# Kernel optimization log

Hardware: AMD Instinct MI355X
Metric: run time of the kernel (lower is better)

## Reference

```python
import jax, jax.numpy as jnp
import numpy as np

N, C, H, E = 4096, 512, 8, 131072
D = C // H
ALPHA = 0.5
EPS = 1e-5


def layer_norm(x, g, b):
    mu = jnp.mean(x, axis=-1, keepdims=True)
    var = jnp.mean((x - mu) ** 2, axis=-1, keepdims=True)
    return (x - mu) * jax.lax.rsqrt(var + EPS) * g + b


def setup_inputs() -> dict:
    key = jax.random.key(0)
    ks = jax.random.split(key, 20)
    s = 0.02
    return {
        "x": jax.random.normal(ks[0], (N, C), jnp.float32),
        "edge_index": jax.random.randint(ks[1], (2, E), 0, N, jnp.int32),
        "local_w": jax.random.normal(ks[2], (C, C), jnp.float32) * s,
        "local_b": jnp.zeros((C,), jnp.float32),
        "in_proj_w": jax.random.normal(ks[3], (3 * C, C), jnp.float32) * s,
        "in_proj_b": jnp.zeros((3 * C,), jnp.float32),
        "attn_out_w": jax.random.normal(ks[4], (C, C), jnp.float32) * s,
        "attn_out_b": jnp.zeros((C,), jnp.float32),
        "output_w": jax.random.normal(ks[5], (C, C), jnp.float32) * s,
        "output_b": jnp.zeros((C,), jnp.float32),
        "norm1_g": jnp.ones((C,), jnp.float32),
        "norm1_b": jnp.zeros((C,), jnp.float32),
        "norm2_g": jnp.ones((C,), jnp.float32),
        "norm2_b": jnp.zeros((C,), jnp.float32),
        "ffn_w1": jax.random.normal(ks[6], (2 * C, C), jnp.float32) * s,
        "ffn_b1": jnp.zeros((2 * C,), jnp.float32),
        "ffn_w2": jax.random.normal(ks[7], (C, 2 * C), jnp.float32) * s,
        "ffn_b2": jnp.zeros((C,), jnp.float32),
    }


def reference(x, edge_index, local_w, local_b, in_proj_w, in_proj_b,
              attn_out_w, attn_out_b, output_w, output_b,
              norm1_g, norm1_b, norm2_g, norm2_b,
              ffn_w1, ffn_b1, ffn_w2, ffn_b2):
    src, dst = edge_index[0], edge_index[1]

    # local branch: linear then scatter-mean over incoming edges
    local_h = x @ local_w.T + local_b                       # [N,C]
    summed = jax.ops.segment_sum(local_h[src], dst, num_segments=N)
    cnt = jax.ops.segment_sum(jnp.ones((E,), x.dtype), dst, num_segments=N)
    local_out = summed / jnp.maximum(cnt, 1.0)[:, None]

    # global branch: full self-attention over all nodes
    qkv = x @ in_proj_w.T + in_proj_b                       # [N,3C]
    q, k, v = jnp.split(qkv, 3, axis=-1)
    q = q.reshape(N, H, D)
    k = k.reshape(N, H, D)
    v = v.reshape(N, H, D)
    scores = jnp.einsum('nhd,mhd->hnm', q, k) / jnp.sqrt(jnp.asarray(D, x.dtype))
    attn = jax.nn.softmax(scores, axis=-1)                  # [H,N,N]
    ctx = jnp.einsum('hnm,mhd->nhd', attn, v).reshape(N, C)
    global_out = ctx @ attn_out_w.T + attn_out_b

    mixed = ALPHA * local_out + (1.0 - ALPHA) * global_out
    hidden = layer_norm(x + (mixed @ output_w.T + output_b), norm1_g, norm1_b)

    ff = jax.nn.gelu(hidden @ ffn_w1.T + ffn_b1, approximate=False) @ ffn_w2.T + ffn_b2
    return layer_norm(hidden + ff, norm2_g, norm2_b)
```

## Files before the change

### kernel.cpp

```cpp
#include <hip/hip_runtime.h>


#define N_NODES 4096
#define C_DIM   512
#define H_HEADS 8
#define D_HEAD  64
#define E_EDGES 131072

typedef unsigned short u16;
typedef unsigned int   u32;
typedef u16   u16x8  __attribute__((ext_vector_type(8)));
typedef __bf16 bf16x8 __attribute__((ext_vector_type(8)));
typedef float  f32x4  __attribute__((ext_vector_type(4)));

__device__ __forceinline__ float b2f(u16 u) {
  unsigned int i = ((unsigned int)u) << 16;
  return __builtin_bit_cast(float, i);
}
__device__ __forceinline__ u16 f2b(float f) {
  unsigned int i = __builtin_bit_cast(unsigned int, f);
  i += 0x7fffu + ((i >> 16) & 1u);
  return (u16)(i >> 16);
}
__device__ __forceinline__ u16 f2b_up(float f) {
  unsigned int i = __builtin_bit_cast(unsigned int, f);
  return (u16)((i + 0x8000u) >> 16);
}
__device__ __forceinline__ void glds16(const u16* g, u16* l) {
  __builtin_amdgcn_global_load_lds(
      (const __attribute__((address_space(1))) void*)g,
      (__attribute__((address_space(3))) void*)l, 16, 0, 0);
}

struct CvtArgs {
  const float* src[7];
  u16* dst[7];
  int n[7];
  int* deg;
};

__global__ __launch_bounds__(256) void cvt_multi(CvtArgs a) {
  const int t = blockIdx.y;
  if (t == 7) {
    const int i = blockIdx.x * 256 + threadIdx.x;
    if (i < N_NODES) a.deg[i] = 0;
    return;
  }
  const int i = (blockIdx.x * 256 + threadIdx.x) * 8;
  if (i >= a.n[t]) return;
  const float* s = a.src[t] + i;
  f32x4 v0 = *(const f32x4*)s;
  f32x4 v1 = *(const f32x4*)(s + 4);
  u16x8 o;
  o[0]=f2b(v0[0]); o[1]=f2b(v0[1]); o[2]=f2b(v0[2]); o[3]=f2b(v0[3]);
  o[4]=f2b(v1[0]); o[5]=f2b(v1[1]); o[6]=f2b(v1[2]); o[7]=f2b(v1[3]);
  *(u16x8*)(a.dst[t] + i) = o;
}

template<int EPI>
__global__ __launch_bounds__(256) void gemm_bt(
    const u16* __restrict__ A, const u16* __restrict__ W,
    const float* __restrict__ bias, void* __restrict__ outp,
    int M, int Nout, int K,
    const float* __restrict__ mloc)
{
  const int tid  = threadIdx.x;
  const int lane = tid & 63, wave = tid >> 6;
  const int quad = lane >> 4, l16 = lane & 15;
  const int wm = wave >> 1, wn = wave & 1;
  const int bm = blockIdx.x, bnb = blockIdx.y;

  __shared__ __align__(16) u16 As[64][128];
  __shared__ __align__(16) u16 Ws[64][128];

  f32x4 acc[2][2] = {};

  const int lr4 = lane >> 4, gs = lane & 15;
  const int g8e = (gs ^ lr4) * 8;
  const int g8o = (gs ^ (4 + lr4)) * 8;
  const u16* aw[8];
#pragma unroll
  for (int c = 0; c < 4; ++c) {
    const int g8 = (c & 1) ? g8o : g8e;
    aw[c]     = A + (size_t)(bm  * 64 + wave * 16 + c * 4 + lr4) * K + g8;
    aw[4 + c] = W + (size_t)(bnb * 64 + wave * 16 + c * 4 + lr4) * K + g8;
  }

  for (int k0 = 0; k0 < K; k0 += 128) {
    __syncthreads();
#pragma unroll
    for (int c = 0; c < 4; ++c) {
      glds16(aw[c] + k0,     &As[wave * 16 + c * 4][0]);
      glds16(aw[4 + c] + k0, &Ws[wave * 16 + c * 4][0]);
    }
    __syncthreads();
#pragma unroll
    for (int ks = 0; ks < 4; ++ks) {
      const int slot = ((ks * 4 + quad) ^ (l16 & 7)) * 8;
      bf16x8 af[2], bf[2];
      af[0] = *(const bf16x8*)&As[wm * 32 +      l16][slot];
      af[1] = *(const bf16x8*)&As[wm * 32 + 16 + l16][slot];
      bf[0] = *(const bf16x8*)&Ws[wn * 32 +      l16][slot];
      bf[1] = *(const bf16x8*)&Ws[wn * 32 + 16 + l16][slot];
#pragma unroll
      for (int i = 0; i < 2; ++i)
#pragma unroll
        for (int j = 0; j < 2; ++j)
          acc[i][j] = __builtin_amdgcn_mfma_f32_16x16x32_bf16(af[i], bf[j], acc[i][j], 0, 0, 0);
    }
  }

#pragma unroll
  for (int i = 0; i < 2; ++i)
#pragma unroll
    for (int j = 0; j < 2; ++j) {
      const int col = bnb * 64 + wn * 32 + j * 16 + l16;
      const float bias_v = bias[col];
#pragma unroll
      for (int r = 0; r < 4; ++r) {
        const int row = bm * 64 + wm * 32 + i * 16 + quad * 4 + r;
        float v = acc[i][j][r] + bias_v;
        const size_t o = (size_t)row * Nout + col;
        if constexpr (EPI == 1) {
          ((float*)outp)[o] = v;
        } else if constexpr (EPI == 2) {
          float gl = 0.5f * v * (1.0f + erff(v * 0.70710678118654752f));
          ((u16*)outp)[o] = f2b(gl);
        } else {
          ((u16*)outp)[o] = f2b(0.5f * mloc[o] + 0.5f * v);
        }
      }
    }
}

__global__ __launch_bounds__(256) void gemm128(
    const u16* __restrict__ A, const u16* __restrict__ W,
    const float* __restrict__ bias0, const float* __restrict__ bias1,
    u16* __restrict__ out0, u16* __restrict__ out1,
    int M, int Nout, int K,
    const int* __restrict__ ei, int* __restrict__ deg)
{
  const int tid  = threadIdx.x;
  if (blockIdx.y == 16) {
#pragma unroll
    for (int i = 0; i < 16; ++i) {
      const int e = blockIdx.x * 4096 + i * 256 + tid;
      atomicAdd(&deg[ei[E_EDGES + e]], 1);
    }
    return;
  }
  const int lane = tid & 63, wave = tid >> 6;
  const int quad = lane >> 4, l16 = lane & 15;
  const int wm = wave >> 1, wn = wave & 1;
  const int bm = blockIdx.x, bnb = blockIdx.y;

  __shared__ __align__(16) u16 As[128][64];
  __shared__ __align__(16) u16 Ws[128][64];

  f32x4 acc[4][4] = {};

  const int lr = lane >> 3, gs = lane & 7;
  const int g8 = (gs ^ lr) * 8;
  const u16* ab = A + (size_t)(bm  * 128 + wave * 32 + lr) * K + g8;
  const u16* wb = W + (size_t)(bnb * 128 + wave * 32 + lr) * K + g8;

  for (int k0 = 0; k0 < K; k0 += 64) {
    __syncthreads();
#pragma unroll
    for (int c = 0; c < 4; ++c) {
      glds16(ab + (size_t)(c * 8) * K + k0, &As[wave * 32 + c * 8][0]);
      glds16(wb + (size_t)(c * 8) * K + k0, &Ws[wave * 32 + c * 8][0]);
    }
    __syncthreads();
#pragma unroll
    for (int ks = 0; ks < 2; ++ks) {
      const int slot = ((ks * 4 + quad) ^ (l16 & 7)) * 8;
      bf16x8 af[4], bf[4];
#pragma unroll
      for (int am = 0; am < 4; ++am)
        af[am] = *(const bf16x8*)&As[wm * 64 + am * 16 + l16][slot];
#pragma unroll
      for (int bn = 0; bn < 4; ++bn)
        bf[bn] = *(const bf16x8*)&Ws[wn * 64 + bn * 16 + l16][slot];
#pragma unroll
      for (int am = 0; am < 4; ++am)
#pragma unroll
        for (int bn = 0; bn < 4; ++bn)
          acc[am][bn] = __builtin_amdgcn_mfma_f32_16x16x32_bf16(af[am], bf[bn], acc[am][bn], 0, 0, 0);
    }
  }

#pragma unroll
  for (int am = 0; am < 4; ++am)
#pragma unroll
    for (int bn = 0; bn < 4; ++bn) {
      const int col = bnb * 128 + wn * 64 + bn * 16 + l16;
      const float bias_v = (col < 512) ? bias0[col] : bias1[col - 512];
#pragma unroll
      for (int r = 0; r < 4; ++r) {
        const int row = bm * 128 + wm * 64 + am * 16 + quad * 4 + r;
        float v = acc[am][bn][r] + bias_v;
        if (col < 512) out0[(size_t)row * 512 + col] = f2b(v);
        else           out1[(size_t)row * 1536 + (col - 512)] = f2b(v);
      }
    }
}

__global__ __launch_bounds__(256) void scan_vtrans(
    const int* __restrict__ deg, int* __restrict__ off, int* __restrict__ cursor,
    const u16* __restrict__ qkv, u16* __restrict__ vt)
{
  if (blockIdx.x == 512) {
    __shared__ int part[256];
    const int t = threadIdx.x;
    int v[16];
    int s = 0;
#pragma unroll
    for (int i = 0; i < 16; ++i) { v[i] = deg[t * 16 + i]; s += v[i]; }
    part[t] = s;
    __syncthreads();
    for (int d = 1; d < 256; d <<= 1) {
      int val = (t >= d) ? part[t - d] : 0;
      __syncthreads();
      if (t >= d) part[t] += val;
      __syncthreads();
    }
    int prefix = (t == 0) ? 0 : part[t - 1];
#pragma unroll
    for (int i = 0; i < 16; ++i) {
      off[t * 16 + i] = prefix;
      cursor[t * 16 + i] = prefix;
      prefix += v[i];
    }
    if (t == 255) off[4096] = prefix;
    return;
  }
  const int tid = threadIdx.x;
  const int d = tid & 63, mg = tid >> 6;
  const int h = blockIdx.x >> 6, mt = blockIdx.x & 63;
  const int m0 = mt * 64 + mg * 16;
  u16 buf[16];
#pragma unroll
  for (int i = 0; i < 16; ++i)
    buf[i] = qkv[(size_t)(m0 + i) * 1536 + 1024 + h * 64 + d];
  u16x8 w0, w1;
#pragma unroll
  for (int i = 0; i < 8; ++i) { w0[i] = buf[i]; w1[i] = buf[8 + i]; }
  u16* op = vt + (size_t)(h * 64 + d) * N_NODES + m0;
  *(u16x8*)op = w0;
  *(u16x8*)(op + 8) = w1;
}

template<int SPLITS>
__global__ __launch_bounds__(256) void attn_kernel(
    const u16* __restrict__ qkv, const u16* __restrict__ vt,
    u16* __restrict__ opart, float* __restrict__ lpart,
    const int* __restrict__ ei, int* __restrict__ cursor, int* __restrict__ csr)
{
  const int tid = threadIdx.x, wave = tid >> 6, lane = tid & 63;
  const int split = blockIdx.z;
  if (split == SPLITS) {
    const int sblk = blockIdx.y * 32 + blockIdx.x;
#pragma unroll
    for (int i = 0; i < 2; ++i) {
      const int e = sblk * 512 + i * 256 + tid;
      const int s = ei[e];
      const int d = ei[E_EDGES + e];
      const int p = atomicAdd(&cursor[d], 1);
      csr[p] = s;
    }
    return;
  }
  const int quad = lane >> 4, l16 = lane & 15;
  const int h = blockIdx.y, tile = blockIdx.x;

  __shared__ __align__(16) u16 Ks[64][64];
  __shared__ __align__(16) u16 Vts[64][64];
  __shared__ __align__(16) u16 Ps[128][72];

  const float QSCALE = 0.18033688011112042f;
  bf16x8 aq[2][2];
#pragma unroll
  for (int mb = 0; mb < 2; ++mb) {
    const int qrow = tile * 128 + wave * 32 + mb * 16 + l16;
    const u16* qp = qkv + (size_t)qrow * 1536 + h * 64 + quad * 8;
    u16x8 q0 = *(const u16x8*)qp;
    u16x8 q1 = *(const u16x8*)(qp + 32);
    u16x8 s0, s1;
#pragma unroll
    for (int i = 0; i < 8; ++i) {
      s0[i] = f2b(b2f(q0[i]) * QSCALE);
      s1[i] = f2b(b2f(q1[i]) * QSCALE);
    }
    aq[mb][0] = __builtin_bit_cast(bf16x8, s0);
    aq[mb][1] = __builtin_bit_cast(bf16x8, s1);
  }

  f32x4 O[2][4] = {};
  float lsum[2][4] = {};

  const int lr = lane >> 3, gs = lane & 7;
  const int g8 = (gs ^ lr) * 8;
  const int R0 = wave * 16 + lr;

  const int mt1 = (split + 1) * (64 / SPLITS);
  for (int mt = split * (64 / SPLITS); mt < mt1; ++mt) {
    __syncthreads();
    glds16(qkv + (size_t)(mt * 64 + R0)     * 1536 + 512 + h * 64 + g8, &Ks[wave * 16][0]);
    glds16(qkv + (size_t)(mt * 64 + R0 + 8) * 1536 + 512 + h * 64 + g8, &Ks[wave * 16 + 8][0]);
    glds16(vt + (size_t)(h * 64 + R0)     * N_NODES + mt * 64 + g8, &Vts[wave * 16][0]);
    glds16(vt + (size_t)(h * 64 + R0 + 8) * N_NODES + mt * 64 + g8, &Vts[wave * 16 + 8][0]);
    __syncthreads();

    f32x4 s[2][4] = {};
#pragma unroll
    for (int ks = 0; ks < 2; ++ks) {
      const int slot = ((ks * 4 + quad) ^ (l16 & 7)) * 8;
      bf16x8 bk[4];
#pragma unroll
      for (int jn = 0; jn < 4; ++jn)
        bk[jn] = *(const bf16x8*)&Ks[jn * 16 + l16][slot];
#pragma unroll
      for (int mb = 0; mb < 2; ++mb)
#pragma unroll
        for (int jn = 0; jn < 4; ++jn)
          s[mb][jn] = __builtin_amdgcn_mfma_f32_16x16x32_bf16(aq[mb][ks], bk[jn], s[mb][jn], 0, 0, 0);
    }

#pragma unroll
    for (int mb = 0; mb < 2; ++mb)
#pragma unroll
      for (int jn = 0; jn < 4; ++jn)
#pragma unroll
        for (int r = 0; r < 4; ++r) {
          float p = __builtin_amdgcn_exp2f(s[mb][jn][r]);
          lsum[mb][r] += p;
          Ps[wave * 32 + mb * 16 + quad * 4 + r][jn * 16 + l16] = f2b_up(p);
        }

#pragma unroll
    for (int ks = 0; ks < 2; ++ks) {
      const int slot = ((ks * 4 + quad) ^ (l16 & 7)) * 8;
      bf16x8 bv[4];
#pragma unroll
      for (int jd = 0; jd < 4; ++jd)
        bv[jd] = *(const bf16x8*)&Vts[jd * 16 + l16][slot];
#pragma unroll
      for (int mb = 0; mb < 2; ++mb) {
        bf16x8 ap = *(const bf16x8*)&Ps[wave * 32 + mb * 16 + l16][ks * 32 + quad * 8];
#pragma unroll
        for (int jd = 0; jd < 4; ++jd)
          O[mb][jd] = __builtin_amdgcn_mfma_f32_16x16x32_bf16(ap, bv[jd], O[mb][jd], 0, 0, 0);
      }
    }
  }

#pragma unroll
  for (int mb = 0; mb < 2; ++mb)
#pragma unroll
    for (int r = 0; r < 4; ++r)
#pragma unroll
      for (int off = 1; off < 16; off <<= 1)
        lsum[mb][r] += __shfl_xor(lsum[mb][r], off);

#pragma unroll
  for (int mb = 0; mb < 2; ++mb)
#pragma unroll
    for (int r = 0; r < 4; ++r) {
      const int row = tile * 128 + wave * 32 + mb * 16 + quad * 4 + r;
      u16* orow = opart + ((size_t)split * N_NODES + row) * C_DIM + h * 64;
#pragma unroll
      for (int jd = 0; jd < 4; ++jd)
        orow[jd * 16 + l16] = f2b(O[mb][jd][r]);
      if (l16 == 0)
        lpart[((size_t)split * N_NODES + row) * H_HEADS + h] = lsum[mb][r];
    }
}

template<int SPLITS>
__global__ __launch_bounds__(256) void combine_gather(
    const u16* __restrict__ opart, const float* __restrict__ lpart,
    u16* __restrict__ ctx,
    const int* __restrict__ off, const int* __restrict__ csr,
    const u16* __restrict__ lh, float* __restrict__ lo)
{
  if (blockIdx.y == 0) {
    const int wave = threadIdx.x >> 6, lane = threadIdx.x & 63;
    const int n = blockIdx.x * 4 + wave;
    const int j0 = off[n], j1 = off[n + 1];
    float acc[8] = {};
    for (int j = j0; j < j1; ++j) {
      const int s = csr[j];
      const u16x8 v = *(const u16x8*)(lh + (size_t)s * C_DIM + lane * 8);
#pragma unroll
      for (int i = 0; i < 8; ++i) acc[i] += b2f(v[i]);
    }
    const float inv = 1.0f / fmaxf((float)(j1 - j0), 1.0f);
    f32x4 o0, o1;
#pragma unroll
    for (int i = 0; i < 4; ++i) { o0[i] = acc[i] * inv; o1[i] = acc[4 + i] * inv; }
    float* op = lo + (size_t)n * C_DIM + lane * 8;
    *(f32x4*)op = o0;
    *(f32x4*)(op + 4) = o1;
    return;
  }
  const size_t base = (size_t)(blockIdx.x * 256 + threadIdx.x) * 8;
  const int row = (int)(base >> 9);
  const int h = (int)((base & 511) >> 6);
  float l = 0.0f;
#pragma unroll
  for (int s = 0; s < SPLITS; ++s)
    l += lpart[(size_t)s * N_NODES * H_HEADS + (size_t)row * H_HEADS + h];
  const float inv = 1.0f / l;
  float o[8] = {};
#pragma unroll
  for (int s = 0; s < SPLITS; ++s) {
    const u16x8 p = *(const u16x8*)(opart + (size_t)s * N_NODES * C_DIM + base);
#pragma unroll
    for (int i = 0; i < 8; ++i) o[i] += b2f(p[i]);
  }
  u16x8 ob;
#pragma unroll
  for (int i = 0; i < 8; ++i) ob[i] = f2b(o[i] * inv);
  *(u16x8*)(ctx + base) = ob;
}

__global__ __launch_bounds__(256) void ln1_kernel(
    const float* __restrict__ x, const float* __restrict__ pr,
    const float* __restrict__ g, const float* __restrict__ b,
    u16* __restrict__ hb, float* __restrict__ hf)
{
  const int wave = threadIdx.x >> 6, lane = threadIdx.x & 63;
  const int row = blockIdx.x * 4 + wave;
  const int c0 = lane * 8;
  const size_t base = (size_t)row * C_DIM + c0;
  f32x4 x0 = *(const f32x4*)(x + base);
  f32x4 x1 = *(const f32x4*)(x + base + 4);
  f32x4 p0 = *(const f32x4*)(pr + base);
  f32x4 p1 = *(const f32x4*)(pr + base + 4);
  float v[8];
#pragma unroll
  for (int i = 0; i < 4; ++i) { v[i] = x0[i] + p0[i]; v[4 + i] = x1[i] + p1[i]; }
  float sum = 0, sq = 0;
#pragma unroll
  for (int i = 0; i < 8; ++i) { sum += v[i]; sq += v[i] * v[i]; }
  for (int off = 1; off < 64; off <<= 1) { sum += __shfl_xor(sum, off); sq += __shfl_xor(sq, off); }
  const float mean = sum * (1.0f / C_DIM);
  const float var  = sq * (1.0f / C_DIM) - mean * mean;
  const float rstd = rsqrtf(var + 1e-5f);
  f32x4 g0 = *(const f32x4*)(g + c0), g1 = *(const f32x4*)(g + c0 + 4);
  f32x4 b0 = *(const f32x4*)(b + c0), b1 = *(const f32x4*)(b + c0 + 4);
  u16x8 ob; f32x4 h0, h1;
#pragma unroll
  for (int i = 0; i < 4; ++i) {
    float hv0 = (v[i]     - mean) * rstd * g0[i] + b0[i];
    float hv1 = (v[4 + i] - mean) * rstd * g1[i] + b1[i];
    h0[i] = hv0; h1[i] = hv1;
    ob[i] = f2b(hv0); ob[4 + i] = f2b(hv1);
  }
  *(u16x8*)(hb + base) = ob;
  *(f32x4*)(hf + base) = h0;
  *(f32x4*)(hf + base + 4) = h1;
}

__global__ __launch_bounds__(256) void ln2_kernel(
    const float* __restrict__ a, const float* __restrict__ c,
    const float* __restrict__ g, const float* __restrict__ b,
    float* __restrict__ out)
{
  const int wave = threadIdx.x >> 6, lane = threadIdx.x & 63;
  const int row = blockIdx.x * 4 + wave;
  const int c0 = lane * 8;
  const size_t base = (size_t)row * C_DIM + c0;
  f32x4 a0 = *(const f32x4*)(a + base), a1 = *(const f32x4*)(a + base + 4);
  f32x4 c0v = *(const f32x4*)(c + base), c1v = *(const f32x4*)(c + base + 4);
  float v[8];
#pragma unroll
  for (int i = 0; i < 4; ++i) { v[i] = a0[i] + c0v[i]; v[4 + i] = a1[i] + c1v[i]; }
  float sum = 0, sq = 0;
#pragma unroll
  for (int i = 0; i < 8; ++i) { sum += v[i]; sq += v[i] * v[i]; }
  for (int off = 1; off < 64; off <<= 1) { sum += __shfl_xor(sum, off); sq += __shfl_xor(sq, off); }
  const float mean = sum * (1.0f / C_DIM);
  const float var  = sq * (1.0f / C_DIM) - mean * mean;
  const float rstd = rsqrtf(var + 1e-5f);
  f32x4 g0 = *(const f32x4*)(g + c0), g1 = *(const f32x4*)(g + c0 + 4);
  f32x4 b0 = *(const f32x4*)(b + c0), b1 = *(const f32x4*)(b + c0 + 4);
  f32x4 h0, h1;
#pragma unroll
  for (int i = 0; i < 4; ++i) {
    h0[i] = (v[i]     - mean) * rstd * g0[i] + b0[i];
    h1[i] = (v[4 + i] - mean) * rstd * g1[i] + b1[i];
  }
  *(f32x4*)(out + base) = h0;
  *(f32x4*)(out + base + 4) = h1;
}

extern "C" void kernel_launch(void* const* d_in, const int* in_sizes, int n_in,
                              void* d_out, int out_size, void* d_ws, size_t ws_size,
                              hipStream_t stream) {
  const float* x          = (const float*)d_in[0];
  const int*   ei         = (const int*)d_in[1];
  const float* local_w    = (const float*)d_in[2];
  const float* local_b    = (const float*)d_in[3];
  const float* in_proj_w  = (const float*)d_in[4];
  const float* in_proj_b  = (const float*)d_in[5];
  const float* attn_out_w = (const float*)d_in[6];
  const float* attn_out_b = (const float*)d_in[7];
  const float* output_w   = (const float*)d_in[8];
  const float* output_b   = (const float*)d_in[9];
  const float* n1g = (const float*)d_in[10];
  const float* n1b = (const float*)d_in[11];
  const float* n2g = (const float*)d_in[12];
  const float* n2b = (const float*)d_in[13];
  const float* ffn_w1 = (const float*)d_in[14];
  const float* ffn_b1 = (const float*)d_in[15];
  const float* ffn_w2 = (const float*)d_in[16];
  const float* ffn_b2 = (const float*)d_in[17];
  float* out = (float*)d_out;

  char* ws = (char*)d_ws;
  size_t o = 0;
  float* local_out = (float*)(ws + o); o += (size_t)N_NODES * C_DIM * 4;
  int* deg    = (int*)(ws + o); o += (N_NODES) * 4;
  int* off    = (int*)(ws + o); o += (N_NODES + 16) * 4;
  int* cursor = (int*)(ws + o); o += (N_NODES) * 4;
  int* csr    = (int*)(ws + o); o += (size_t)E_EDGES * 4;
  u16* xb   = (u16*)(ws + o); o += (size_t)N_NODES * C_DIM * 2;
  u16* wbLQ = (u16*)(ws + o); o += (size_t)4 * C_DIM * C_DIM * 2;
  u16* wbA  = (u16*)(ws + o); o += (size_t)C_DIM * C_DIM * 2;
  u16* wbO  = (u16*)(ws + o); o += (size_t)C_DIM * C_DIM * 2;
  u16* wbF1 = (u16*)(ws + o); o += (size_t)2 * C_DIM * C_DIM * 2;
  u16* wbF2 = (u16*)(ws + o); o += (size_t)2 * C_DIM * C_DIM * 2;
  u16* local_h   = (u16*)(ws + o); o += (size_t)N_NODES * C_DIM * 2;
  u16* qkvb      = (u16*)(ws + o); o += (size_t)N_NODES * 3 * C_DIM * 2;
  u16* ctxb      = (u16*)(ws + o); o += (size_t)N_NODES * C_DIM * 2;
  u16* mixed     = (u16*)(ws + o); o += (size_t)N_NODES * C_DIM * 2;
  u16* hidden_bf = (u16*)(ws + o); o += (size_t)N_NODES * C_DIM * 2;
  float* hidden_f = (float*)(ws + o); o += (size_t)N_NODES * C_DIM * 4;
  u16* ff1       = (u16*)(ws + o); o += (size_t)N_NODES * 2 * C_DIM * 2;
  float* proj  = (float*)qkvb;
  float* ff2   = (float*)local_out;
  u16*   vt    = xb;
  u16* opart4 = (u16*)(ws + o);
  float* lpart4 = (float*)(ws + o + (size_t)4 * N_NODES * C_DIM * 2);
  const size_t need4 = o + (size_t)4 * N_NODES * C_DIM * 2 + (size_t)4 * N_NODES * H_HEADS * 4;
  const bool use4 = (ws_size >= need4);
  u16* opart2 = (u16*)hidden_bf;
  float* lpart2 = (float*)(opart2 + (size_t)2 * N_NODES * C_DIM);

  CvtArgs ca;
  ca.src[0] = x;          ca.dst[0] = xb;   ca.n[0] = N_NODES * C_DIM;
  ca.src[1] = local_w;    ca.dst[1] = wbLQ;                  ca.n[1] = C_DIM * C_DIM;
  ca.src[2] = in_proj_w;  ca.dst[2] = wbLQ + C_DIM * C_DIM;  ca.n[2] = 3 * C_DIM * C_DIM;
  ca.src[3] = attn_out_w; ca.dst[3] = wbA;  ca.n[3] = C_DIM * C_DIM;
  ca.src[4] = output_w;   ca.dst[4] = wbO;  ca.n[4] = C_DIM * C_DIM;
  ca.src[5] = ffn_w1;     ca.dst[5] = wbF1; ca.n[5] = 2 * C_DIM * C_DIM;
  ca.src[6] = ffn_w2;     ca.dst[6] = wbF2; ca.n[6] = 2 * C_DIM * C_DIM;
  ca.deg = deg;
  cvt_multi<<<dim3(N_NODES * C_DIM / 2048, 8), 256, 0, stream>>>(ca);

  gemm128<<<dim3(32, 17), 256, 0, stream>>>(xb, wbLQ, local_b, in_proj_b,
      local_h, qkvb, N_NODES, 4 * C_DIM, C_DIM, ei, deg);

  scan_vtrans<<<513, 256, 0, stream>>>(deg, off, cursor, qkvb, vt);

  if (use4) {
    attn_kernel<4><<<dim3(32, 8, 5), 256, 0, stream>>>(qkvb, vt, opart4, lpart4,
        ei, cursor, csr);
    combine_gather<4><<<dim3(1024, 2), 256, 0, stream>>>(opart4, lpart4, ctxb,
        off, csr, local_h, local_out);
  } else {
    attn_kernel<2><<<dim3(32, 8, 3), 256, 0, stream>>>(qkvb, vt, opart2, lpart2,
        ei, cursor, csr);
    combine_gather<2><<<dim3(1024, 2), 256, 0, stream>>>(opart2, lpart2, ctxb,
        off, csr, local_h, local_out);
  }

  gemm_bt<3><<<dim3(64, 8), 256, 0, stream>>>(ctxb, wbA, attn_out_b, mixed,
      N_NODES, C_DIM, C_DIM, local_out);

  gemm_bt<1><<<dim3(64, 8), 256, 0, stream>>>(mixed, wbO, output_b, proj,
      N_NODES, C_DIM, C_DIM, nullptr);
  ln1_kernel<<<N_NODES / 4, 256, 0, stream>>>(x, proj, n1g, n1b, hidden_bf, hidden_f);

  gemm_bt<2><<<dim3(64, 16), 256, 0, stream>>>(hidden_bf, wbF1, ffn_b1, ff1,
      N_NODES, 2 * C_DIM, C_DIM, nullptr);
  gemm_bt<1><<<dim3(64, 8), 256, 0, stream>>>(ff1, wbF2, ffn_b2, ff2,
      N_NODES, C_DIM, 2 * C_DIM, nullptr);
  ln2_kernel<<<N_NODES / 4, 256, 0, stream>>>(hidden_f, ff2, n2g, n2b, out);
}
```

Measured before the change: 264.7 us.

## Double-buffer K/V tiles and keep P in registers via permlane swaps

```diff
diff --git a/kernel.cpp b/kernel.cpp
--- a/kernel.cpp
+++ b/kernel.cpp
@@ -12,6 +12,7 @@
 typedef u16   u16x8  __attribute__((ext_vector_type(8)));
 typedef __bf16 bf16x8 __attribute__((ext_vector_type(8)));
 typedef float  f32x4  __attribute__((ext_vector_type(4)));
+typedef u32    u32x4  __attribute__((ext_vector_type(4)));
 
 __device__ __forceinline__ float b2f(u16 u) {
   unsigned int i = ((unsigned int)u) << 16;
@@ -22,9 +23,16 @@
   i += 0x7fffu + ((i >> 16) & 1u);
   return (u16)(i >> 16);
 }
-__device__ __forceinline__ u16 f2b_up(float f) {
-  unsigned int i = __builtin_bit_cast(unsigned int, f);
-  return (u16)((i + 0x8000u) >> 16);
+__device__ __forceinline__ u32 cvtpk(float lo, float hi) {
+  u32 r;
+  asm("v_cvt_pk_bf16_f32 %0, %1, %2" : "=v"(r) : "v"(lo), "v"(hi));
+  return r;
+}
+__device__ __forceinline__ void pl32swap(u32& x, u32& y) {
+  asm("v_permlane32_swap_b32 %0, %1" : "+v"(x), "+v"(y));
+}
+__device__ __forceinline__ void pl16swap(u32& x, u32& y) {
+  asm("v_permlane16_swap_b32 %0, %1" : "+v"(x), "+v"(y));
 }
 __device__ __forceinline__ void glds16(const u16* g, u16* l) {
   __builtin_amdgcn_global_load_lds(
@@ -274,9 +282,8 @@
   const int quad = lane >> 4, l16 = lane & 15;
   const int h = blockIdx.y, tile = blockIdx.x;
 
-  __shared__ __align__(16) u16 Ks[64][64];
-  __shared__ __align__(16) u16 Vts[64][64];
-  __shared__ __align__(16) u16 Ps[128][72];
+  __shared__ __align__(16) u16 Ks[2][64][64];
+  __shared__ __align__(16) u16 Vts[2][64][64];
 
   const float QSCALE = 0.18033688011112042f;
   bf16x8 aq[2][2];
@@ -297,74 +304,106 @@
   }
 
   f32x4 O[2][4] = {};
-  float lsum[2][4] = {};
+  float lsum[2] = {};
 
   const int lr = lane >> 3, gs = lane & 7;
   const int g8 = (gs ^ lr) * 8;
   const int R0 = wave * 16 + lr;
 
-  const int mt1 = (split + 1) * (64 / SPLITS);
-  for (int mt = split * (64 / SPLITS); mt < mt1; ++mt) {
-    __syncthreads();
-    glds16(qkv + (size_t)(mt * 64 + R0)     * 1536 + 512 + h * 64 + g8, &Ks[wave * 16][0]);
-    glds16(qkv + (size_t)(mt * 64 + R0 + 8) * 1536 + 512 + h * 64 + g8, &Ks[wave * 16 + 8][0]);
-    glds16(vt + (size_t)(h * 64 + R0)     * N_NODES + mt * 64 + g8, &Vts[wave * 16][0]);
-    glds16(vt + (size_t)(h * 64 + R0 + 8) * N_NODES + mt * 64 + g8, &Vts[wave * 16 + 8][0]);
-    __syncthreads();
-
-    f32x4 s[2][4] = {};
+  const u16* kp = qkv + (size_t)R0 * 1536 + 512 + h * 64 + g8;
+  const u16* vp = vt + (size_t)(h * 64 + R0) * N_NODES + g8;
+
+  const int mt0 = split * (64 / SPLITS), mt1 = (split + 1) * (64 / SPLITS);
+
+  {
+    const size_t ko = (size_t)mt0 * 64 * 1536;
+    glds16(kp + ko,            &Ks[0][wave * 16][0]);
+    glds16(kp + ko + 8 * 1536, &Ks[0][wave * 16 + 8][0]);
+    glds16(vp + mt0 * 64,                        &Vts[0][wave * 16][0]);
+    glds16(vp + mt0 * 64 + 8 * N_NODES,          &Vts[0][wave * 16 + 8][0]);
+  }
+
+  for (int mt = mt0; mt < mt1; ++mt) {
+    const int cur = (mt - mt0) & 1;
+    if (mt + 1 < mt1) {
+      const size_t ko = (size_t)(mt + 1) * 64 * 1536;
+      glds16(kp + ko,            &Ks[cur ^ 1][wave * 16][0]);
+      glds16(kp + ko + 8 * 1536, &Ks[cur ^ 1][wave * 16 + 8][0]);
+      glds16(vp + (mt + 1) * 64,                 &Vts[cur ^ 1][wave * 16][0]);
+      glds16(vp + (mt + 1) * 64 + 8 * N_NODES,   &Vts[cur ^ 1][wave * 16 + 8][0]);
+      asm volatile("s_waitcnt vmcnt(4)" ::: "memory");
+    } else {
+      asm volatile("s_waitcnt vmcnt(0)" ::: "memory");
+    }
+    __builtin_amdgcn_s_barrier();
+    __builtin_amdgcn_sched_barrier(0);
+
+    f32x4 st[2][4] = {};
+    __builtin_amdgcn_s_setprio(1);
 #pragma unroll
     for (int ks = 0; ks < 2; ++ks) {
       const int slot = ((ks * 4 + quad) ^ (l16 & 7)) * 8;
-      bf16x8 bk[4];
+      bf16x8 af[4];
 #pragma unroll
       for (int jn = 0; jn < 4; ++jn)
-        bk[jn] = *(const bf16x8*)&Ks[jn * 16 + l16][slot];
+        af[jn] = *(const bf16x8*)&Ks[cur][jn * 16 + l16][slot];
 #pragma unroll
       for (int mb = 0; mb < 2; ++mb)
 #pragma unroll
         for (int jn = 0; jn < 4; ++jn)
-          s[mb][jn] = __builtin_amdgcn_mfma_f32_16x16x32_bf16(aq[mb][ks], bk[jn], s[mb][jn], 0, 0, 0);
-    }
-
-#pragma unroll
-    for (int mb = 0; mb < 2; ++mb)
-#pragma unroll
-      for (int jn = 0; jn < 4; ++jn)
-#pragma unroll
-        for (int r = 0; r < 4; ++r) {
-          float p = __builtin_amdgcn_exp2f(s[mb][jn][r]);
-          lsum[mb][r] += p;
-          Ps[wave * 32 + mb * 16 + quad * 4 + r][jn * 16 + l16] = f2b_up(p);
-        }
-
+          st[mb][jn] = __builtin_amdgcn_mfma_f32_16x16x32_bf16(af[jn], aq[mb][ks], st[mb][jn], 0, 0, 0);
+    }
+    __builtin_amdgcn_s_setprio(0);
+
+    bf16x8 pa[2][2];
+#pragma unroll
+    for (int mb = 0; mb < 2; ++mb) {
+      u32 pk[4][2];
+#pragma unroll
+      for (int jn = 0; jn < 4; ++jn) {
+        float p0 = __builtin_amdgcn_exp2f(st[mb][jn][0]);
+        float p1 = __builtin_amdgcn_exp2f(st[mb][jn][1]);
+        float p2 = __builtin_amdgcn_exp2f(st[mb][jn][2]);
+        float p3 = __builtin_amdgcn_exp2f(st[mb][jn][3]);
+        lsum[mb] += (p0 + p1) + (p2 + p3);
+        pk[jn][0] = cvtpk(p0, p1);
+        pk[jn][1] = cvtpk(p2, p3);
+      }
+#pragma unroll
+      for (int ks = 0; ks < 2; ++ks) {
+        u32 x0 = pk[2 * ks][0], y0 = pk[2 * ks + 1][0];
+        u32 x1 = pk[2 * ks][1], y1 = pk[2 * ks + 1][1];
+        pl32swap(x0, y0); pl16swap(x0, y0);
+        pl32swap(x1, y1); pl16swap(x1, y1);
+        u32x4 av;
+        av[0] = x0; av[1] = x1; av[2] = y0; av[3] = y1;
+        pa[mb][ks] = __builtin_bit_cast(bf16x8, av);
+      }
+    }
+
+    __builtin_amdgcn_s_setprio(1);
 #pragma unroll
     for (int ks = 0; ks < 2; ++ks) {
       const int slot = ((ks * 4 + quad) ^ (l16 & 7)) * 8;
       bf16x8 bv[4];
 #pragma unroll
       for (int jd = 0; jd < 4; ++jd)
-        bv[jd] = *(const bf16x8*)&Vts[jd * 16 + l16][slot];
-#pragma unroll
-      for (int mb = 0; mb < 2; ++mb) {
-        bf16x8 ap = *(const bf16x8*)&Ps[wave * 32 + mb * 16 + l16][ks * 32 + quad * 8];
+        bv[jd] = *(const bf16x8*)&Vts[cur][jd * 16 + l16][slot];
+#pragma unroll
+      for (int mb = 0; mb < 2; ++mb)
 #pragma unroll
         for (int jd = 0; jd < 4; ++jd)
-          O[mb][jd] = __builtin_amdgcn_mfma_f32_16x16x32_bf16(ap, bv[jd], O[mb][jd], 0, 0, 0);
-      }
-    }
-  }
-
-#pragma unroll
-  for (int mb = 0; mb < 2; ++mb)
-#pragma unroll
-    for (int r = 0; r < 4; ++r)
-#pragma unroll
-      for (int off = 1; off < 16; off <<= 1)
-        lsum[mb][r] += __shfl_xor(lsum[mb][r], off);
-
-#pragma unroll
-  for (int mb = 0; mb < 2; ++mb)
+          O[mb][jd] = __builtin_amdgcn_mfma_f32_16x16x32_bf16(pa[mb][ks], bv[jd], O[mb][jd], 0, 0, 0);
+    }
+    __builtin_amdgcn_s_setprio(0);
+    __builtin_amdgcn_s_barrier();
+  }
+
+#pragma unroll
+  for (int mb = 0; mb < 2; ++mb) {
+    float ls = lsum[mb];
+    ls += __shfl_xor(ls, 16);
+    ls += __shfl_xor(ls, 32);
 #pragma unroll
     for (int r = 0; r < 4; ++r) {
       const int row = tile * 128 + wave * 32 + mb * 16 + quad * 4 + r;
@@ -372,9 +411,12 @@
 #pragma unroll
       for (int jd = 0; jd < 4; ++jd)
         orow[jd * 16 + l16] = f2b(O[mb][jd][r]);
-      if (l16 == 0)
-        lpart[((size_t)split * N_NODES + row) * H_HEADS + h] = lsum[mb][r];
-    }
+    }
+    if (lane < 16) {
+      const int row = tile * 128 + wave * 32 + mb * 16 + l16;
+      lpart[((size_t)split * N_NODES + row) * H_HEADS + h] = ls;
+    }
+  }
 }
 
 template<int SPLITS>
```

Result: faster. 255.2 us (-3.6%).
